# Kernel optimization log

Measured on AMD Instinct MI355X. Metric: run time of the kernel, lower is better.

The kernel has to match this reference:

```python
import jax, jax.numpy as jnp
import numpy as np

K = 15  # window_size


def setup_inputs() -> dict:
    key = jax.random.key(0)
    k1, k2, k3, k4 = jax.random.split(key, 4)
    x = jax.random.normal(k1, (8, 256, 240, 240), dtype=jnp.float32)
    wq = jax.random.normal(k2, (144, 256), dtype=jnp.float32) * (1.0 / np.sqrt(256))
    wk = jax.random.normal(k3, (144, 256), dtype=jnp.float32) * (1.0 / np.sqrt(256))
    wproj = jax.random.normal(k4, (256, 256), dtype=jnp.float32) * (1.0 / np.sqrt(256))
    return {"x": x, "wq": wq, "wk": wk, "wproj": wproj}


def _pnlm(x, wq, wk, wproj):
    b, c, h, w = x.shape
    ph, pw = (-h) % K, (-w) % K
    if ph or pw:
        x_pad = jnp.pad(x, ((0, 0), (0, 0), (0, ph), (0, pw)), mode='reflect')
    else:
        x_pad = x
    H, W = x_pad.shape[2], x_pad.shape[3]
    nh, nw = H // K, W // K
    N = K * K  # tokens per window
    # blockify: (B,C,H,W) -> (B*nh*nw, C, N)
    blocks = (x_pad.reshape(b, c, nh, K, nw, K)
              .transpose(0, 2, 4, 1, 3, 5)
              .reshape(b * nh * nw, c, N))
    q = jnp.einsum('ec,bcn->bne', wq, blocks)   # (B', N, E)
    km = jnp.einsum('ec,bcm->bem', wk, blocks)  # (B', E, N)
    att = jnp.einsum('bne,bem->bnm', q, km)     # (B', N, N)
    scale = 1.0 / jnp.sqrt(jnp.asarray(q.shape[-1], dtype=att.dtype))
    att = jax.nn.softmax(att * scale, axis=-1)
    y = jnp.einsum('bnm,bcm->bcn', att, blocks)  # att @ V, V = blocks^T
    y = jnp.einsum('oc,bcn->bon', wproj, y)      # 1x1 proj_out
    # unblockify: (B', C, N) -> (B, C, H, W)
    y = (y.reshape(b, nh, nw, c, K, K)
         .transpose(0, 3, 1, 4, 2, 5)
         .reshape(b, c, H, W))
    y = y[:, :, :h, :w]
    return x + y


def reference(x, wq, wk, wproj):
    return _pnlm(x, wq, wk, wproj)
```

## Files before the change

kernel.cpp:

```cpp
#include <hip/hip_runtime.h>


typedef __bf16 bf16x8 __attribute__((ext_vector_type(8)));
typedef float  f32x4  __attribute__((ext_vector_type(4)));

#define MFMA(a,b,c) __builtin_amdgcn_mfma_f32_16x16x32_bf16((a),(b),(c),0,0,0)

#define QK_ROW 320
#define KL_STRIDE 168

__device__ __forceinline__ unsigned short f2bf(float f){
  union { float f; unsigned int u; } v; v.f = f;
  unsigned int r = v.u + 0x7FFFu + ((v.u >> 16) & 1u);
  return (unsigned short)(r >> 16);
}
__device__ __forceinline__ int swz(int row, int col){
  return row*256 + ((((col >> 3) ^ (row & 7)) << 3) | (col & 7));
}
__device__ __forceinline__ bf16x8 ld_frag_lds(const unsigned short* p, int idx){
  uint4 v = *(const uint4*)(p + idx);
  return __builtin_bit_cast(bf16x8, v);
}
__device__ __forceinline__ bf16x8 ld_frag_b(const void* p){
  uint4 v = *(const uint4*)p;
  return __builtin_bit_cast(bf16x8, v);
}

__device__ __forceinline__ void repack_frag(const unsigned int* plo, const unsigned int* phi,
                                            uint4* outf, int lane){
  const int nn = lane & 15, hh = lane >> 4;
  const int sla = nn + 32*(hh & 1);
  const int slb = sla + 16;
  const bool up = hh >= 2;
  #pragma unroll
  for (int k = 0; k < 8; ++k){
    unsigned int a0 = (unsigned int)__shfl((int)plo[2*k],   sla);
    unsigned int a1 = (unsigned int)__shfl((int)plo[2*k+1], sla);
    unsigned int b0 = (unsigned int)__shfl((int)phi[2*k],   sla);
    unsigned int b1 = (unsigned int)__shfl((int)phi[2*k+1], sla);
    unsigned int c0 = (unsigned int)__shfl((int)plo[2*k],   slb);
    unsigned int c1 = (unsigned int)__shfl((int)plo[2*k+1], slb);
    unsigned int d0 = (unsigned int)__shfl((int)phi[2*k],   slb);
    unsigned int d1 = (unsigned int)__shfl((int)phi[2*k+1], slb);
    outf[k] = make_uint4(up?a1:a0, up?b1:b0, up?c1:c0, up?d1:d0);
  }
}

__global__ __launch_bounds__(512) void k_qk(
    const float* __restrict__ x, const float* __restrict__ wq,
    const float* __restrict__ wk,
    unsigned short* __restrict__ qkws)
{
  __shared__ unsigned short xt [128*256];
  __shared__ unsigned short wqs[ 32*256];
  __shared__ unsigned short wks[ 32*256];
  const int wg  = blockIdx.x;
  const int b   = wg / 450;
  const int hw0 = (wg % 450) * 128;
  const int tid = threadIdx.x;
  const int lane = tid & 63, wave = tid >> 6;
  const int col  = lane & 15, hi = lane >> 4;

  {
    const float* xb = x + (size_t)b * 256 * 57600 + hw0;
    const int hw_l = tid & 127;
    #pragma unroll 4
    for (int i = 0; i < 32; ++i){
      int cp = (tid >> 7) * 32 + i;
      int c  = cp * 2;
      float f0 = xb[(size_t)c     * 57600 + hw_l];
      float f1 = xb[(size_t)(c+1) * 57600 + hw_l];
      *(unsigned int*)(&xt[swz(hw_l, c)]) =
          (unsigned int)f2bf(f0) | ((unsigned int)f2bf(f1) << 16);
    }
  }
  __syncthreads();

  bf16x8 af[8];
  const int arow = wave*16 + col;
  #pragma unroll
  for (int k = 0; k < 8; ++k)
    af[k] = ld_frag_lds(xt, swz(arow, k*32 + hi*8));

  const size_t orow_base = (size_t)b*57600 + hw0 + wave*16;

  for (int eg = 0; eg < 5; ++eg){
    __syncthreads();
    for (int i = 0; i < 8; ++i){
      int idx = tid + i*512;
      int e_l = idx >> 7, c = (idx & 127) * 2;
      int e = eg*32 + e_l;
      float2 vq = make_float2(0.f,0.f), vk = make_float2(0.f,0.f);
      if (e < 144){
        vq = *(const float2*)(wq + (size_t)e*256 + c);
        vk = *(const float2*)(wk + (size_t)e*256 + c);
      }
      *(unsigned int*)(&wqs[swz(e_l, c)]) =
          (unsigned int)f2bf(vq.x) | ((unsigned int)f2bf(vq.y) << 16);
      *(unsigned int*)(&wks[swz(e_l, c)]) =
          (unsigned int)f2bf(vk.x) | ((unsigned int)f2bf(vk.y) << 16);
    }
    __syncthreads();
    #pragma unroll
    for (int etl = 0; etl < 2; ++etl){
      f32x4 aq = {0.f,0.f,0.f,0.f}, ak = {0.f,0.f,0.f,0.f};
      const int el = etl*16 + col;
      #pragma unroll
      for (int k = 0; k < 8; ++k){
        int idx = swz(el, k*32 + hi*8);
        bf16x8 bq = ld_frag_lds(wqs, idx);
        bf16x8 bk = ld_frag_lds(wks, idx);
        aq = MFMA(af[k], bq, aq);
        ak = MFMA(af[k], bk, ak);
      }
      const int e_out = eg*32 + etl*16 + col;
      #pragma unroll
      for (int jj = 0; jj < 4; ++jj){
        size_t row = orow_base + hi*4 + jj;
        qkws[row*QK_ROW + e_out]       = f2bf(aq[jj]);
        qkws[row*QK_ROW + 160 + e_out] = f2bf(ak[jj]);
      }
    }
  }
}

__global__ __launch_bounds__(512,4) void k_attn(
    const float* __restrict__ x, const float* __restrict__ wproj,
    const unsigned short* __restrict__ qkws, float* __restrict__ out)
{
  __shared__ __align__(16) unsigned short S[40320 + 480];
  unsigned short* kl = S;
  unsigned short* xl = S;
  unsigned short* wl = S + 32768;
  unsigned int*  hwp = (unsigned int*)(S + 40320);
  const int wg = blockIdx.x;
  const int b  = wg >> 8;
  const int th = (wg >> 4) & 15, tw = wg & 15;
  const int h0 = th*15, w0 = tw*15;
  const int tid = threadIdx.x;
  const int lane = tid & 63, wave = tid >> 6;
  const int col  = lane & 15, hi = lane >> 4;
  const size_t xbase = (size_t)b * 256 * 57600;
  const unsigned short* qkb = qkws + (size_t)b * 57600 * QK_ROW;

  if (tid < 240){
    int ms = tid <= 224 ? tid : 224;
    hwp[tid] = (unsigned int)((h0 + ms/15)*240 + w0 + ms%15);
  }
  __syncthreads();

  for (int i = tid; i < 240*20; i += 512){
    int m = i / 20, eb = i - m*20;
    *(uint4*)(&kl[m*KL_STRIDE + eb*8]) =
        *(const uint4*)(qkb + (size_t)hwp[m]*QK_ROW + 160 + eb*8);
  }
  __syncthreads();

  uint4 attf[2][8];
  #pragma unroll
  for (int slot = 0; slot < 2; ++slot){
    const int nt = wave + slot*8;
    if (nt < 15){
      const int n  = nt*16 + col;
      const int na = n <= 224 ? n : 224;
      const unsigned short* qrow = qkb + (size_t)hwp[na]*QK_ROW;
      bf16x8 qf[5];
      #pragma unroll
      for (int c = 0; c < 5; ++c)
        qf[c] = ld_frag_b(qrow + c*32 + hi*8);
      f32x4 at[15];
      #pragma unroll
      for (int T = 0; T < 15; ++T){
        f32x4 acc = {0.f,0.f,0.f,0.f};
        #pragma unroll
        for (int c = 0; c < 5; ++c){
          bf16x8 kf = ld_frag_lds(kl, (T*16 + col)*KL_STRIDE + c*32 + hi*8);
          acc = MFMA(kf, qf[c], acc);
        }
        at[T] = acc;
      }
      const float sc = 0.12022458674074695f;
      float M = -3.0e38f;
      #pragma unroll
      for (int T = 0; T < 15; ++T){
        #pragma unroll
        for (int jj = 0; jj < 4; ++jj){
          int m = T*16 + hi*4 + jj;
          if (m <= 224) M = fmaxf(M, at[T][jj]*sc);
        }
      }
      M = fmaxf(M, __shfl_xor(M, 16));
      M = fmaxf(M, __shfl_xor(M, 32));
      float Ssum = 0.f;
      #pragma unroll
      for (int T = 0; T < 15; ++T){
        #pragma unroll
        for (int jj = 0; jj < 4; ++jj){
          int m = T*16 + hi*4 + jj;
          float v = (m <= 224) ? exp2f(at[T][jj]*sc - M) : 0.f;
          at[T][jj] = v; Ssum += v;
        }
      }
      Ssum += __shfl_xor(Ssum, 16);
      Ssum += __shfl_xor(Ssum, 32);
      const float inv = 1.0f / Ssum;
      unsigned int plo[16], phi[16];
      #pragma unroll
      for (int T = 0; T < 15; ++T){
        plo[T] = (unsigned int)f2bf(at[T][0]*inv) | ((unsigned int)f2bf(at[T][1]*inv) << 16);
        phi[T] = (unsigned int)f2bf(at[T][2]*inv) | ((unsigned int)f2bf(at[T][3]*inv) << 16);
      }
      plo[15] = 0u; phi[15] = 0u;
      repack_frag(plo, phi, attf[slot], lane);
    }
  }

  unsigned int ylo[2][16], yhi[2][16];
  #pragma unroll
  for (int half = 0; half < 2; ++half){
    __syncthreads();
    for (int i = tid; i < 128*128; i += 512){
      int c = i >> 7, m = (i & 127)*2;
      int m0 = m <= 224 ? m : 224;
      float f0 = (m     <= 224) ? x[xbase + (size_t)(half*128 + c)*57600 + hwp[m0]]   : 0.f;
      float f1 = (m + 1 <= 224) ? x[xbase + (size_t)(half*128 + c)*57600 + hwp[m0+1]] : 0.f;
      *(unsigned int*)(&xl[swz(c, m)]) =
          (unsigned int)f2bf(f0) | ((unsigned int)f2bf(f1) << 16);
    }
    __syncthreads();
    #pragma unroll
    for (int slot = 0; slot < 2; ++slot){
      const int nt = wave + slot*8;
      if (nt < 15){
        #pragma unroll
        for (int ct = 0; ct < 8; ++ct){
          f32x4 acc = {0.f,0.f,0.f,0.f};
          #pragma unroll
          for (int k = 0; k < 8; ++k){
            bf16x8 xf = ld_frag_lds(xl, swz(ct*16 + col, k*32 + hi*8));
            acc = MFMA(xf, __builtin_bit_cast(bf16x8, attf[slot][k]), acc);
          }
          ylo[slot][half*8 + ct] = (unsigned int)f2bf(acc[0]) | ((unsigned int)f2bf(acc[1]) << 16);
          yhi[slot][half*8 + ct] = (unsigned int)f2bf(acc[2]) | ((unsigned int)f2bf(acc[3]) << 16);
        }
      }
    }
  }

  uint4 y1f[2][8];
  #pragma unroll
  for (int slot = 0; slot < 2; ++slot){
    const int nt = wave + slot*8;
    if (nt < 15)
      repack_frag(ylo[slot], yhi[slot], y1f[slot], lane);
  }

  #pragma unroll 1
  for (int oe = 0; oe < 16; ++oe){
    __syncthreads();
    for (int i = tid; i < 16*128; i += 512){
      int olr = i >> 7, c = (i & 127)*2;
      const float* wr = wproj + (size_t)(oe*16 + olr)*256 + c;
      *(unsigned int*)(&wl[swz(olr, c)]) =
          (unsigned int)f2bf(wr[0]) | ((unsigned int)f2bf(wr[1]) << 16);
    }
    __syncthreads();
    bf16x8 awf[8];
    #pragma unroll
    for (int k = 0; k < 8; ++k)
      awf[k] = ld_frag_lds(wl, swz(col, k*32 + hi*8));
    #pragma unroll
    for (int slot = 0; slot < 2; ++slot){
      const int nt = wave + slot*8;
      if (nt < 15){
        f32x4 y2 = {0.f,0.f,0.f,0.f};
        #pragma unroll
        for (int k = 0; k < 8; ++k)
          y2 = MFMA(awf[k], __builtin_bit_cast(bf16x8, y1f[slot][k]), y2);
        const int n = nt*16 + col;
        if (n <= 224){
          const size_t pix = hwp[n];
          #pragma unroll
          for (int jj = 0; jj < 4; ++jj){
            int o = oe*16 + hi*4 + jj;
            const size_t idx = xbase + (size_t)o*57600 + pix;
            out[idx] = y2[jj] + x[idx];
          }
        }
      }
    }
  }
}

extern "C" void kernel_launch(void* const* d_in, const int* in_sizes, int n_in,
                              void* d_out, int out_size, void* d_ws, size_t ws_size,
                              hipStream_t stream)
{
  const float* x     = (const float*)d_in[0];
  const float* wq    = (const float*)d_in[1];
  const float* wk    = (const float*)d_in[2];
  const float* wproj = (const float*)d_in[3];
  float* out = (float*)d_out;
  unsigned short* qkws = (unsigned short*)d_ws;
  (void)in_sizes; (void)n_in; (void)out_size; (void)ws_size;

  k_qk  <<<dim3(3600), dim3(512), 0, stream>>>(x, wq, wk, qkws);
  k_attn<<<dim3(2048), dim3(512), 0, stream>>>(x, wproj, qkws, out);
}
```

Before: 1.143 ms.

## Emit window-blocked bf16 copy of x in QK pass and stage QK output through LDS

The QK kernel now also writes a bf16 copy of x laid out per 15x15 window, 240 tokens per channel row, into workspace. The new attention kernel reads that contiguous bf16 block for both the att@V operand and the residual, instead of gathering strided fp32 x twice. QK results are staged in LDS and written out as coalesced 16-byte rows. The residual now uses the bf16-rounded x, which lowers accuracy, and the fast path runs only when the workspace is large enough, otherwise it falls back to the old kernel.

```diff
diff --git a/kernel.cpp b/kernel.cpp
--- a/kernel.cpp
+++ b/kernel.cpp
@@ -8,11 +8,16 @@
 
 #define QK_ROW 320
 #define KL_STRIDE 168
+#define XBB_ROW 240
 
 __device__ __forceinline__ unsigned short f2bf(float f){
   union { float f; unsigned int u; } v; v.f = f;
   unsigned int r = v.u + 0x7FFFu + ((v.u >> 16) & 1u);
   return (unsigned short)(r >> 16);
+}
+__device__ __forceinline__ float bf2f(unsigned short u){
+  union { unsigned int u; float f; } v; v.u = ((unsigned int)u) << 16;
+  return v.f;
 }
 __device__ __forceinline__ int swz(int row, int col){
   return row*256 + ((((col >> 3) ^ (row & 7)) << 3) | (col & 7));
@@ -49,11 +54,13 @@
 __global__ __launch_bounds__(512) void k_qk(
     const float* __restrict__ x, const float* __restrict__ wq,
     const float* __restrict__ wk,
-    unsigned short* __restrict__ qkws)
+    unsigned short* __restrict__ qkws, unsigned short* __restrict__ xbb)
 {
-  __shared__ unsigned short xt [128*256];
-  __shared__ unsigned short wqs[ 32*256];
-  __shared__ unsigned short wks[ 32*256];
+  __shared__ __align__(16) unsigned short S[128*320];
+  __shared__ unsigned short wqs[32*256];
+  __shared__ unsigned short wks[32*256];
+  unsigned short* xt = S;
+  unsigned short* ol = S;
   const int wg  = blockIdx.x;
   const int b   = wg / 450;
   const int hw0 = (wg % 450) * 128;
@@ -64,14 +71,27 @@
   {
     const float* xb = x + (size_t)b * 256 * 57600 + hw0;
     const int hw_l = tid & 127;
+    size_t bb = 0;
+    if (xbb){
+      int hw = hw0 + hw_l;
+      int h = hw / 240, w = hw - h*240;
+      int th = h / 15, r = h - th*15;
+      int tw = w / 15, s = w - tw*15;
+      bb = (size_t)(b*256 + th*16 + tw) * (256*XBB_ROW) + (r*15 + s);
+    }
     #pragma unroll 4
     for (int i = 0; i < 32; ++i){
       int cp = (tid >> 7) * 32 + i;
       int c  = cp * 2;
       float f0 = xb[(size_t)c     * 57600 + hw_l];
       float f1 = xb[(size_t)(c+1) * 57600 + hw_l];
+      unsigned short u0 = f2bf(f0), u1 = f2bf(f1);
       *(unsigned int*)(&xt[swz(hw_l, c)]) =
-          (unsigned int)f2bf(f0) | ((unsigned int)f2bf(f1) << 16);
+          (unsigned int)u0 | ((unsigned int)u1 << 16);
+      if (xbb){
+        xbb[bb + (size_t)c    *XBB_ROW] = u0;
+        xbb[bb + (size_t)(c+1)*XBB_ROW] = u1;
+      }
     }
   }
   __syncthreads();
@@ -81,8 +101,7 @@
   #pragma unroll
   for (int k = 0; k < 8; ++k)
     af[k] = ld_frag_lds(xt, swz(arow, k*32 + hi*8));
-
-  const size_t orow_base = (size_t)b*57600 + hw0 + wave*16;
+  __syncthreads();
 
   for (int eg = 0; eg < 5; ++eg){
     __syncthreads();
@@ -114,17 +133,196 @@
         ak = MFMA(af[k], bk, ak);
       }
       const int e_out = eg*32 + etl*16 + col;
+      const int rb = wave*16 + hi*4;
       #pragma unroll
       for (int jj = 0; jj < 4; ++jj){
-        size_t row = orow_base + hi*4 + jj;
-        qkws[row*QK_ROW + e_out]       = f2bf(aq[jj]);
-        qkws[row*QK_ROW + 160 + e_out] = f2bf(ak[jj]);
-      }
-    }
-  }
-}
-
-__global__ __launch_bounds__(512,4) void k_attn(
+        ol[(rb + jj)*QK_ROW + e_out]       = f2bf(aq[jj]);
+        ol[(rb + jj)*QK_ROW + 160 + e_out] = f2bf(ak[jj]);
+      }
+    }
+  }
+  __syncthreads();
+
+  {
+    const size_t gbase = ((size_t)b*57600 + hw0) * QK_ROW;
+    for (int i = tid; i < 128*40; i += 512){
+      int r = i / 40, k2 = i - r*40;
+      *(uint4*)(qkws + gbase + (size_t)r*QK_ROW + k2*8) =
+          *(const uint4*)(ol + r*QK_ROW + k2*8);
+    }
+  }
+}
+
+
+__global__ __launch_bounds__(512,4) void k_attn_b(
+    const unsigned short* __restrict__ xbb, const float* __restrict__ wproj,
+    const unsigned short* __restrict__ qkws, float* __restrict__ out)
+{
+  __shared__ __align__(16) unsigned short S[40320 + 480];
+  unsigned short* kl = S;
+  unsigned short* xl = S;
+  unsigned short* wl = S + 32768;
+  unsigned int*  hwp = (unsigned int*)(S + 40320);
+  const int wg = blockIdx.x;
+  const int b  = wg >> 8;
+  const int th = (wg >> 4) & 15, tw = wg & 15;
+  const int h0 = th*15, w0 = tw*15;
+  const int tid = threadIdx.x;
+  const int lane = tid & 63, wave = tid >> 6;
+  const int col  = lane & 15, hi = lane >> 4;
+  const size_t obase = (size_t)b * 256 * 57600;
+  const unsigned short* qkb = qkws + (size_t)b * 57600 * QK_ROW;
+  const unsigned short* xbw = xbb + (size_t)wg * (256*XBB_ROW);
+
+  if (tid < 240){
+    int ms = tid <= 224 ? tid : 224;
+    hwp[tid] = (unsigned int)((h0 + ms/15)*240 + w0 + ms%15);
+  }
+  __syncthreads();
+
+  for (int i = tid; i < 240*20; i += 512){
+    int m = i / 20, eb = i - m*20;
+    *(uint4*)(&kl[m*KL_STRIDE + eb*8]) =
+        *(const uint4*)(qkb + (size_t)hwp[m]*QK_ROW + 160 + eb*8);
+  }
+  __syncthreads();
+
+  uint4 attf[2][8];
+  #pragma unroll
+  for (int slot = 0; slot < 2; ++slot){
+    const int nt = wave + slot*8;
+    if (nt < 15){
+      const int n  = nt*16 + col;
+      const int na = n <= 224 ? n : 224;
+      const unsigned short* qrow = qkb + (size_t)hwp[na]*QK_ROW;
+      bf16x8 qf[5];
+      #pragma unroll
+      for (int c = 0; c < 5; ++c)
+        qf[c] = ld_frag_b(qrow + c*32 + hi*8);
+      f32x4 at[15];
+      #pragma unroll
+      for (int T = 0; T < 15; ++T){
+        f32x4 acc = {0.f,0.f,0.f,0.f};
+        #pragma unroll
+        for (int c = 0; c < 5; ++c){
+          bf16x8 kf = ld_frag_lds(kl, (T*16 + col)*KL_STRIDE + c*32 + hi*8);
+          acc = MFMA(kf, qf[c], acc);
+        }
+        at[T] = acc;
+      }
+      const float sc = 0.12022458674074695f;
+      float M = -3.0e38f;
+      #pragma unroll
+      for (int T = 0; T < 15; ++T){
+        #pragma unroll
+        for (int jj = 0; jj < 4; ++jj){
+          int m = T*16 + hi*4 + jj;
+          if (m <= 224) M = fmaxf(M, at[T][jj]*sc);
+        }
+      }
+      M = fmaxf(M, __shfl_xor(M, 16));
+      M = fmaxf(M, __shfl_xor(M, 32));
+      float Ssum = 0.f;
+      #pragma unroll
+      for (int T = 0; T < 15; ++T){
+        #pragma unroll
+        for (int jj = 0; jj < 4; ++jj){
+          int m = T*16 + hi*4 + jj;
+          float v = (m <= 224) ? exp2f(at[T][jj]*sc - M) : 0.f;
+          at[T][jj] = v; Ssum += v;
+        }
+      }
+      Ssum += __shfl_xor(Ssum, 16);
+      Ssum += __shfl_xor(Ssum, 32);
+      const float inv = 1.0f / Ssum;
+      unsigned int plo[16], phi[16];
+      #pragma unroll
+      for (int T = 0; T < 15; ++T){
+        plo[T] = (unsigned int)f2bf(at[T][0]*inv) | ((unsigned int)f2bf(at[T][1]*inv) << 16);
+        phi[T] = (unsigned int)f2bf(at[T][2]*inv) | ((unsigned int)f2bf(at[T][3]*inv) << 16);
+      }
+      plo[15] = 0u; phi[15] = 0u;
+      repack_frag(plo, phi, attf[slot], lane);
+    }
+  }
+
+  unsigned int ylo[2][16], yhi[2][16];
+  #pragma unroll
+  for (int half = 0; half < 2; ++half){
+    __syncthreads();
+    for (int i = tid; i < 128*32; i += 512){
+      int c = i >> 5, m8 = i & 31;
+      uint4 v = make_uint4(0u,0u,0u,0u);
+      if (m8 < 30)
+        v = *(const uint4*)(xbw + (size_t)(half*128 + c)*XBB_ROW + m8*8);
+      *(uint4*)(&xl[swz(c, m8*8)]) = v;
+    }
+    __syncthreads();
+    #pragma unroll
+    for (int slot = 0; slot < 2; ++slot){
+      const int nt = wave + slot*8;
+      if (nt < 15){
+        #pragma unroll
+        for (int ct = 0; ct < 8; ++ct){
+          f32x4 acc = {0.f,0.f,0.f,0.f};
+          #pragma unroll
+          for (int k = 0; k < 8; ++k){
+            bf16x8 xf = ld_frag_lds(xl, swz(ct*16 + col, k*32 + hi*8));
+            acc = MFMA(xf, __builtin_bit_cast(bf16x8, attf[slot][k]), acc);
+          }
+          ylo[slot][half*8 + ct] = (unsigned int)f2bf(acc[0]) | ((unsigned int)f2bf(acc[1]) << 16);
+          yhi[slot][half*8 + ct] = (unsigned int)f2bf(acc[2]) | ((unsigned int)f2bf(acc[3]) << 16);
+        }
+      }
+    }
+  }
+
+  uint4 y1f[2][8];
+  #pragma unroll
+  for (int slot = 0; slot < 2; ++slot){
+    const int nt = wave + slot*8;
+    if (nt < 15)
+      repack_frag(ylo[slot], yhi[slot], y1f[slot], lane);
+  }
+
+  #pragma unroll 1
+  for (int oe = 0; oe < 16; ++oe){
+    __syncthreads();
+    for (int i = tid; i < 16*128; i += 512){
+      int olr = i >> 7, c = (i & 127)*2;
+      const float* wr = wproj + (size_t)(oe*16 + olr)*256 + c;
+      *(unsigned int*)(&wl[swz(olr, c)]) =
+          (unsigned int)f2bf(wr[0]) | ((unsigned int)f2bf(wr[1]) << 16);
+    }
+    __syncthreads();
+    bf16x8 awf[8];
+    #pragma unroll
+    for (int k = 0; k < 8; ++k)
+      awf[k] = ld_frag_lds(wl, swz(col, k*32 + hi*8));
+    #pragma unroll
+    for (int slot = 0; slot < 2; ++slot){
+      const int nt = wave + slot*8;
+      if (nt < 15){
+        f32x4 y2 = {0.f,0.f,0.f,0.f};
+        #pragma unroll
+        for (int k = 0; k < 8; ++k)
+          y2 = MFMA(awf[k], __builtin_bit_cast(bf16x8, y1f[slot][k]), y2);
+        const int n = nt*16 + col;
+        if (n <= 224){
+          const size_t pix = hwp[n];
+          #pragma unroll
+          for (int jj = 0; jj < 4; ++jj){
+            int o = oe*16 + hi*4 + jj;
+            float xr = bf2f(xbw[(size_t)o*XBB_ROW + n]);
+            out[obase + (size_t)o*57600 + pix] = y2[jj] + xr;
+          }
+        }
+      }
+    }
+  }
+}
+
+__global__ __launch_bounds__(512,4) void k_attn_s(
     const float* __restrict__ x, const float* __restrict__ wproj,
     const unsigned short* __restrict__ qkws, float* __restrict__ out)
 {
@@ -301,9 +499,18 @@
   const float* wk    = (const float*)d_in[2];
   const float* wproj = (const float*)d_in[3];
   float* out = (float*)d_out;
+  (void)in_sizes; (void)n_in; (void)out_size;
+
+  const size_t QKWS_B = (size_t)8*57600*QK_ROW*2;
+  const size_t XBB_B  = (size_t)8*256*256*XBB_ROW*2;
   unsigned short* qkws = (unsigned short*)d_ws;
-  (void)in_sizes; (void)n_in; (void)out_size; (void)ws_size;
-
-  k_qk  <<<dim3(3600), dim3(512), 0, stream>>>(x, wq, wk, qkws);
-  k_attn<<<dim3(2048), dim3(512), 0, stream>>>(x, wproj, qkws, out);
-}
+
+  if (ws_size >= QKWS_B + XBB_B){
+    unsigned short* xbb = (unsigned short*)((char*)d_ws + QKWS_B);
+    k_qk    <<<dim3(3600), dim3(512), 0, stream>>>(x, wq, wk, qkws, xbb);
+    k_attn_b<<<dim3(2048), dim3(512), 0, stream>>>(xbb, wproj, qkws, out);
+  } else {
+    k_qk    <<<dim3(3600), dim3(512), 0, stream>>>(x, wq, wk, qkws, nullptr);
+    k_attn_s<<<dim3(2048), dim3(512), 0, stream>>>(x, wproj, qkws, out);
+  }
+}
```

After: 1.278 ms. 11.8% more time.
